# Kernel tuning notes

Measured on AMD Instinct MI355X. Metric: run time of the kernel, lower is better.

## Reference

```python
import jax, jax.numpy as jnp
import numpy as np

# MACE/molgym-style SimpleModel with max_ell=1, hidden_irreps = 64x0e + 64x1o,
# num_interactions=2, num_elements=10, num_bessel=8, polynomial cutoff p=5, r_max=5.0.
N, E, C, NE, NB, H = 20000, 320000, 64, 10, 8, 64
R_MAX = 5.0
P_CUT = 5


def _mlp(x, W1, W2, W3):
    # radial MLP producing per-edge tensor-product weights (silu nonlinearity)
    h = jax.nn.silu(x @ W1)
    h = jax.nn.silu(h @ W2)
    return h @ W3


def setup_inputs() -> dict:
    key = jax.random.key(0)
    ks = jax.random.split(key, 24)
    positions = jax.random.normal(ks[0], (N, 3), jnp.float32)
    edge_index = jax.random.randint(ks[1], (2, E), 0, N)
    shifts = jnp.zeros((E, 3), jnp.float32)
    species = jax.random.randint(ks[2], (N,), 0, NE)
    node_attrs = jax.nn.one_hot(species, NE, dtype=jnp.float32)

    def w(k, shape, fan_in):
        return jax.random.normal(k, shape, jnp.float32) / np.sqrt(fan_in)

    params = dict(
        W_embed=w(ks[3], (NE, C), NE),
        R1_W1=w(ks[4], (NB, H), NB), R1_W2=w(ks[5], (H, H), H), R1_W3=w(ks[6], (H, 2 * C), H),
        U1_s=w(ks[7], (C, C), C),
        L1_s=w(ks[8], (C, C), C), L1_v=w(ks[9], (C, C), C),
        K1_s=w(ks[10], (C, NE, C), C * NE),
        R2_W1=w(ks[11], (NB, H), NB), R2_W2=w(ks[12], (H, H), H), R2_W3=w(ks[13], (H, 4 * C), H),
        U2_s=w(ks[14], (C, C), C), U2_v=w(ks[15], (C, C), C),
        L2_s=w(ks[16], (2 * C, C), 2 * C), L2_v=w(ks[17], (2 * C, C), 2 * C),
        K2_s=w(ks[18], (C, NE, C), C * NE), K2_v=w(ks[19], (C, NE, C), C * NE),
    )
    return dict(positions=positions, node_attrs=node_attrs, edge_index=edge_index,
                shifts=shifts, **params)


def _forward(positions, node_attrs, shifts, W_embed,
             R1_W1, R1_W2, R1_W3, U1_s, L1_s, L1_v, K1_s,
             R2_W1, R2_W2, R2_W3, U2_s, U2_v, L2_s, L2_v, K2_s, K2_v,
             edge_index):
    snd, rcv = edge_index[0], edge_index[1]
    # edge vectors / lengths
    vec = positions[snd] - positions[rcv] + shifts            # [E,3]
    length = jnp.sqrt(jnp.sum(vec * vec, axis=1, keepdims=True) + 1e-12)  # [E,1]
    unit = vec / length
    # spherical harmonics (normalize=True, component normalization): Y0=1, Y1=sqrt(3)*r_hat
    Y1 = np.float32(np.sqrt(3.0)) * unit                      # [E,3]
    # Bessel radial basis * polynomial cutoff
    n = jnp.arange(1, NB + 1, dtype=jnp.float32)
    bessel = np.float32(np.sqrt(2.0 / R_MAX)) * jnp.sin(n * np.float32(np.pi) * length / R_MAX) / length
    u = length / R_MAX
    p = P_CUT
    poly = (1.0 - 0.5 * (p + 1) * (p + 2) * u ** p
            + p * (p + 2) * u ** (p + 1)
            - 0.5 * p * (p + 1) * u ** (p + 2))
    edge_feats = bessel * (poly * (u < 1.0))                  # [E,NB]
    # node embedding (linear on one-hot species)
    s0 = node_attrs @ W_embed                                 # [N,C]

    # ---- interaction block 1 (input feats: scalars only) ----
    s = s0 @ U1_s                                             # linear_up
    tpw = _mlp(edge_feats, R1_W1, R1_W2, R1_W3).reshape(E, 2, C)
    s_e = s[snd]                                              # gather sender feats
    m_s = tpw[:, 0] * s_e                                     # 0e x 0e -> 0e  [E,C]
    m_v = (tpw[:, 1] * s_e)[:, :, None] * Y1[:, None, :]      # 0e x 1o -> 1o  [E,C,3]
    agg_s = jax.ops.segment_sum(m_s, rcv, num_segments=N)
    agg_v = jax.ops.segment_sum(m_v, rcv, num_segments=N)
    skip_s = jnp.einsum('nu,nv,uvd->nd', s0, node_attrs, K1_s)  # skip tensor product
    s1 = agg_s @ L1_s + skip_s                                # [N,C]
    v1 = jnp.einsum('nci,cd->ndi', agg_v, L1_v)               # [N,C,3]

    # ---- interaction block 2 (input feats: 64x0e + 64x1o) ----
    s = s1 @ U2_s
    v = jnp.einsum('nci,cd->ndi', v1, U2_v)
    tpw = _mlp(edge_feats, R2_W1, R2_W2, R2_W3).reshape(E, 4, C)
    s_e, v_e = s[snd], v[snd]
    mA = tpw[:, 0] * s_e                                      # 0e x 0e -> 0e
    mB = (tpw[:, 1] * s_e)[:, :, None] * Y1[:, None, :]       # 0e x 1o -> 1o
    mC = tpw[:, 2][:, :, None] * v_e                          # 1o x 0e -> 1o
    mD = tpw[:, 3] * (jnp.einsum('eci,ei->ec', v_e, Y1) / np.float32(np.sqrt(3.0)))  # 1o x 1o -> 0e
    mid_s = jnp.concatenate([mA, mD], axis=1)                 # [E,2C]
    mid_v = jnp.concatenate([mB, mC], axis=1)                 # [E,2C,3]
    agg_s = jax.ops.segment_sum(mid_s, rcv, num_segments=N)
    agg_v = jax.ops.segment_sum(mid_v, rcv, num_segments=N)
    skip_s = jnp.einsum('nu,nv,uvd->nd', s1, node_attrs, K2_s)
    skip_v = jnp.einsum('nui,nv,uvd->ndi', v1, node_attrs, K2_v)
    s2 = agg_s @ L2_s + skip_s                                # [N,C]
    v2 = jnp.einsum('nci,cd->ndi', agg_v, L2_v) + skip_v      # [N,C,3]
    return jnp.concatenate([s2, v2.reshape(N, 3 * C)], axis=1)  # [N,4C]


def reference(positions, node_attrs, edge_index, shifts, W_embed,
              R1_W1, R1_W2, R1_W3, U1_s, L1_s, L1_v, K1_s,
              R2_W1, R2_W2, R2_W3, U2_s, U2_v, L2_s, L2_v, K2_s, K2_v):
    return _forward(positions, node_attrs, shifts, W_embed,
                    R1_W1, R1_W2, R1_W3, U1_s, L1_s, L1_v, K1_s,
                    R2_W1, R2_W2, R2_W3, U2_s, U2_v, L2_s, L2_v, K2_s, K2_v,
                    edge_index)
```

## Files before the change

### kernel.cpp

```cpp
#include <hip/hip_runtime.h>
#include <hip/hip_fp16.h>

#define NNODES 20000
#define NEDGES 320000
#define NELEM  10
#define NC     (NNODES * 64)

#define OFF_SUP1 ((size_t)0)
#define OFF_AGS1 ((size_t)1 * NC)
#define OFF_AGV1 ((size_t)2 * NC)
#define OFF_AGS2 ((size_t)0)
#define OFF_AGV2 ((size_t)2 * NC)
#define OFF_SUP2 ((size_t)8 * NC)
#define OFF_VUP2 ((size_t)9 * NC)
#define OFF_SKS2 ((size_t)12 * NC)
#define OFF_SKV2 ((size_t)13 * NC)
#define OFF_INT  ((size_t)16 * NC)

#define SMEM_BYTES 38656

typedef __attribute__((ext_vector_type(8))) short bf16x8;
typedef __attribute__((ext_vector_type(4))) float f32x4;

__device__ __forceinline__ float silu(float x) { return x / (1.0f + __expf(-x)); }
__device__ __forceinline__ int rfl(int v) { return __builtin_amdgcn_readfirstlane(v); }
__device__ __forceinline__ int rl_i(int v, int l) { return __builtin_amdgcn_readlane(v, l); }
__device__ __forceinline__ float rl_f(float v, int l) {
    return __int_as_float(__builtin_amdgcn_readlane(__float_as_int(v), l));
}
__device__ __forceinline__ uint2 split2(float x0, float x1) {
    unsigned int b0 = __float_as_uint(x0), b1 = __float_as_uint(x1);
    unsigned int h0 = (b0 + 0x7FFF + ((b0 >> 16) & 1)) & 0xFFFF0000u;
    unsigned int h1 = (b1 + 0x7FFF + ((b1 >> 16) & 1)) & 0xFFFF0000u;
    unsigned int l0 = __float_as_uint(x0 - __uint_as_float(h0));
    unsigned int l1 = __float_as_uint(x1 - __uint_as_float(h1));
    unsigned int hi = (h0 >> 16) | (h1 & 0xFFFF0000u);
    unsigned int lo = ((l0 + 0x7FFF + ((l0 >> 16) & 1)) >> 16)
                    | ((l1 + 0x7FFF + ((l1 >> 16) & 1)) & 0xFFFF0000u);
    return make_uint2(hi, lo);
}

__global__ __launch_bounds__(256) void k_wsplit(
    const float* __restrict__ W3a, const float* __restrict__ W3b,
    unsigned short* __restrict__ out)
{
    int t = blockIdx.x * 256 + threadIdx.x;
    float x; unsigned short *ph, *pl; int idx;
    if (t < 8192) {
        int n = t >> 6, k = t & 63;
        x = W3a[k * 128 + n]; ph = out; pl = out + 8192; idx = n * 64 + k;
    } else {
        int u = t - 8192; int n = u >> 6, k = u & 63;
        x = W3b[k * 256 + n]; ph = out + 16384; pl = out + 32768; idx = n * 64 + k;
    }
    unsigned int b = __float_as_uint(x);
    unsigned int h = (b + 0x7FFF + ((b >> 16) & 1)) & 0xFFFF0000u;
    unsigned int r = __float_as_uint(x - __uint_as_float(h));
    ph[idx] = (unsigned short)(h >> 16);
    pl[idx] = (unsigned short)((r + 0x7FFF + ((r >> 16) & 1)) >> 16);
}

__global__ __launch_bounds__(256) void k_hist(const int* __restrict__ eidx,
                                              int* __restrict__ hist)
{
    int e = blockIdx.x * 256 + threadIdx.x;
    atomicAdd(&hist[eidx[NEDGES + e]], 1);
}

__global__ __launch_bounds__(1024) void k_scan(const int* __restrict__ hist,
                                               int* __restrict__ cursor)
{
    __shared__ int wsum[16];
    __shared__ int gbase;
    int tid = threadIdx.x;
    int lane = tid & 63, wvid = tid >> 6;
    if (tid == 0) gbase = 0;
    __syncthreads();
    for (int seg = 0; seg < 20; ++seg) {
        int i = seg * 1024 + tid;
        int v = (i < NNODES) ? hist[i] : 0;
        int s = v;
        #pragma unroll
        for (int d = 1; d < 64; d <<= 1) {
            int t = __shfl_up(s, d, 64);
            if (lane >= d) s += t;
        }
        if (lane == 63) wsum[wvid] = s;
        __syncthreads();
        if (wvid == 0) {
            int w = (lane < 16) ? wsum[lane] : 0;
            #pragma unroll
            for (int d = 1; d < 16; d <<= 1) {
                int t = __shfl_up(w, d, 64);
                if (lane >= d) w += t;
            }
            if (lane < 16) wsum[lane] = w;
        }
        __syncthreads();
        int wbase = (wvid == 0) ? 0 : wsum[wvid - 1];
        if (i < NNODES) cursor[i] = gbase + wbase + s - v;
        int segtot = wsum[15];
        __syncthreads();
        if (tid == 0) gbase += segtot;
    }
}

__global__ __launch_bounds__(256) void k_scatter(const int* __restrict__ eidx,
                                                 int* __restrict__ cursor,
                                                 int* __restrict__ sorted)
{
    int e = blockIdx.x * 256 + threadIdx.x;
    int pos = atomicAdd(&cursor[eidx[NEDGES + e]], 1);
    sorted[pos] = e;
}

__global__ __launch_bounds__(256) void k_node_pre(
    const float* __restrict__ attrs, const float* __restrict__ Wemb,
    const float* __restrict__ U1s, __half* __restrict__ sUp1)
{
    int lane = threadIdx.x & 63, wv = threadIdx.x >> 6;
    int n = blockIdx.x * 4 + wv;
    __shared__ __align__(16) float s0sh[4][64];
    float s0 = 0.f;
    #pragma unroll
    for (int v = 0; v < NELEM; ++v) s0 += attrs[n * NELEM + v] * Wemb[v * 64 + lane];
    s0sh[wv][lane] = s0;
    __syncthreads();
    float a = 0.f;
    #pragma unroll 8
    for (int k = 0; k < 64; ++k) a += s0sh[wv][k] * U1s[k * 64 + lane];
    sUp1[n * 64 + lane] = __float2half_rn(a);
}

__global__ __launch_bounds__(256, 4) void k_edge1(
    const float* __restrict__ pos, const int* __restrict__ eidx,
    const float* __restrict__ shf, const int* __restrict__ sorted,
    const float* __restrict__ W1, const float* __restrict__ W2,
    const unsigned short* __restrict__ w3h, const unsigned short* __restrict__ w3l,
    const __half* __restrict__ sUp1,
    float* __restrict__ agS1, float* __restrict__ agV1)
{
    __shared__ __align__(16) char smem[SMEM_BYTES];
    float (*ysh)[3]   = (float (*)[3])(smem);
    int*  ssh         = (int*)(smem + 768);
    int*  rsh         = (int*)(smem + 1024);
    float (*h1sh)[65] = (float (*)[65])(smem + 1280);
    unsigned short (*h2buf)[64][72] = (unsigned short (*)[64][72])(smem + 17920);
    float (*fsh)[9]   = (float (*)[9])(smem + 36352);

    const int tid = threadIdx.x;
    const int lane = tid & 63;
    const int w = rfl(tid >> 6);
    const int e0 = blockIdx.x * 64;

    {
        int e = tid >> 2, sub = tid & 3;
        int sid = sorted[e0 + e];
        int snd = eidx[sid], rcv = eidx[NEDGES + sid];
        float dx = pos[snd * 3 + 0] - pos[rcv * 3 + 0] + shf[(size_t)sid * 3 + 0];
        float dy = pos[snd * 3 + 1] - pos[rcv * 3 + 1] + shf[(size_t)sid * 3 + 1];
        float dz = pos[snd * 3 + 2] - pos[rcv * 3 + 2] + shf[(size_t)sid * 3 + 2];
        float len = sqrtf(dx * dx + dy * dy + dz * dz + 1e-12f);
        float inv = 1.0f / len;
        float u = len * 0.2f;
        float u2 = u * u, u4 = u2 * u2, u5 = u4 * u, u6 = u5 * u, u7 = u6 * u;
        float cut = (u < 1.0f) ? (1.0f - 21.0f * u5 + 35.0f * u6 - 15.0f * u7) : 0.0f;
        float s = 0.632455532033676f * inv * cut;
        #pragma unroll
        for (int kk = 0; kk < 2; ++kk) {
            int k = sub * 2 + kk;
            fsh[e][k] = s * sinf((float)(k + 1) * 0.628318530717959f * len);
        }
        if (sub == 0) {
            ssh[e] = snd; rsh[e] = rcv;
            ysh[e][0] = 1.73205080756888f * dx * inv;
            ysh[e][1] = 1.73205080756888f * dy * inv;
            ysh[e][2] = 1.73205080756888f * dz * inv;
        }
    }
    __syncthreads();

    const int rAll = rsh[lane];
    const int sAll = ssh[lane];
    const float y0A = ysh[lane][0], y1A = ysh[lane][1], y2A = ysh[lane][2];

    {
        float f[8];
        #pragma unroll
        for (int k = 0; k < 8; ++k) f[k] = fsh[lane][k];
        const float* __restrict__ w1b = W1 + w * 16;
        #pragma unroll
        for (int j = 0; j < 16; ++j) {
            float a = 0.f;
            #pragma unroll
            for (int k = 0; k < 8; ++k) a = fmaf(f[k], w1b[k * 64 + j], a);
            h1sh[lane][w * 16 + j] = silu(a);
        }
    }
    __syncthreads();

    {
        const float2* __restrict__ w2b = (const float2*)W2 + w * 8;
        float2 acc[8];
        #pragma unroll
        for (int j = 0; j < 8; ++j) acc[j] = make_float2(0.f, 0.f);
        for (int k = 0; k < 64; ++k) {
            float h = h1sh[lane][k];
            const float2* __restrict__ wk = w2b + k * 32;
            #pragma unroll
            for (int j = 0; j < 8; ++j) {
                float2 wv = wk[j];
                acc[j].x = fmaf(h, wv.x, acc[j].x);
                acc[j].y = fmaf(h, wv.y, acc[j].y);
            }
        }
        #pragma unroll
        for (int j = 0; j < 8; ++j) {
            uint2 p = split2(silu(acc[j].x), silu(acc[j].y));
            *(unsigned int*)&h2buf[0][lane][w * 16 + 2 * j] = p.x;
            *(unsigned int*)&h2buf[1][lane][w * 16 + 2 * j] = p.y;
        }
    }
    __syncthreads();

    const int q = lane >> 4, nl = lane & 15;
    float* trw = (float*)(smem + 1280) + w * 1024;

    const unsigned short* ar = &h2buf[0][w * 16 + nl][0];
    const unsigned short* al = &h2buf[1][w * 16 + nl][0];
    bf16x8 ah0 = *(const bf16x8*)(ar + q * 8);
    bf16x8 ah1 = *(const bf16x8*)(ar + 32 + q * 8);
    bf16x8 al0 = *(const bf16x8*)(al + q * 8);
    bf16x8 al1 = *(const bf16x8*)(al + 32 + q * 8);

    float sreg[16];
    #pragma unroll
    for (int i = 0; i < 16; ++i)
        sreg[i] = __half2float(sUp1[rl_i(sAll, w * 16 + i) * 64 + lane]);

    #pragma unroll
    for (int nt = 0; nt < 4; ++nt) {
        int c = nt * 16 + nl;
        const unsigned short* wh = w3h + c * 64 + q * 8;
        const unsigned short* wl = w3l + c * 64 + q * 8;
        bf16x8 bh0 = *(const bf16x8*)wh;
        bf16x8 bh1 = *(const bf16x8*)(wh + 32);
        bf16x8 bl0 = *(const bf16x8*)wl;
        bf16x8 bl1 = *(const bf16x8*)(wl + 32);
        f32x4 a = {0.f, 0.f, 0.f, 0.f};
        a = __builtin_amdgcn_mfma_f32_16x16x32_bf16(ah0, bh0, a, 0, 0, 0);
        a = __builtin_amdgcn_mfma_f32_16x16x32_bf16(ah1, bh1, a, 0, 0, 0);
        a = __builtin_amdgcn_mfma_f32_16x16x32_bf16(ah0, bl0, a, 0, 0, 0);
        a = __builtin_amdgcn_mfma_f32_16x16x32_bf16(ah1, bl1, a, 0, 0, 0);
        a = __builtin_amdgcn_mfma_f32_16x16x32_bf16(al0, bh0, a, 0, 0, 0);
        a = __builtin_amdgcn_mfma_f32_16x16x32_bf16(al1, bh1, a, 0, 0, 0);
        #pragma unroll
        for (int r = 0; r < 4; ++r) {
            int li = q * 4 + r;
            trw[li * 64 + ((c + 4 * li) & 63)] = a[r];
        }
    }
    {
        float accS = 0.f;
        int cur = rl_i(rAll, w * 16);
        #pragma unroll
        for (int i = 0; i < 16; ++i) {
            int e = w * 16 + i;
            int rcv = rl_i(rAll, e);
            if (rcv != cur) {
                unsafeAtomicAdd(&agS1[cur * 64 + lane], accS);
                accS = 0.f; cur = rcv;
            }
            accS += trw[i * 64 + ((lane + 4 * i) & 63)] * sreg[i];
        }
        unsafeAtomicAdd(&agS1[cur * 64 + lane], accS);
    }

    #pragma unroll
    for (int nt = 0; nt < 4; ++nt) {
        int c = nt * 16 + nl;
        int ng = 64 + c;
        const unsigned short* wh = w3h + ng * 64 + q * 8;
        const unsigned short* wl = w3l + ng * 64 + q * 8;
        bf16x8 bh0 = *(const bf16x8*)wh;
        bf16x8 bh1 = *(const bf16x8*)(wh + 32);
        bf16x8 bl0 = *(const bf16x8*)wl;
        bf16x8 bl1 = *(const bf16x8*)(wl + 32);
        f32x4 a = {0.f, 0.f, 0.f, 0.f};
        a = __builtin_amdgcn_mfma_f32_16x16x32_bf16(ah0, bh0, a, 0, 0, 0);
        a = __builtin_amdgcn_mfma_f32_16x16x32_bf16(ah1, bh1, a, 0, 0, 0);
        a = __builtin_amdgcn_mfma_f32_16x16x32_bf16(ah0, bl0, a, 0, 0, 0);
        a = __builtin_amdgcn_mfma_f32_16x16x32_bf16(ah1, bl1, a, 0, 0, 0);
        a = __builtin_amdgcn_mfma_f32_16x16x32_bf16(al0, bh0, a, 0, 0, 0);
        a = __builtin_amdgcn_mfma_f32_16x16x32_bf16(al1, bh1, a, 0, 0, 0);
        #pragma unroll
        for (int r = 0; r < 4; ++r) {
            int li = q * 4 + r;
            trw[li * 64 + ((c + 4 * li) & 63)] = a[r];
        }
    }
    {
        float b0 = 0.f, b1 = 0.f, b2 = 0.f;
        int cur = rl_i(rAll, w * 16);
        #pragma unroll
        for (int i = 0; i < 16; ++i) {
            int e = w * 16 + i;
            int rcv = rl_i(rAll, e);
            if (rcv != cur) {
                unsafeAtomicAdd(&agV1[cur * 192 +       lane], b0);
                unsafeAtomicAdd(&agV1[cur * 192 +  64 + lane], b1);
                unsafeAtomicAdd(&agV1[cur * 192 + 128 + lane], b2);
                b0 = b1 = b2 = 0.f; cur = rcv;
            }
            float msg = trw[i * 64 + ((lane + 4 * i) & 63)] * sreg[i];
            b0 += msg * rl_f(y0A, e);
            b1 += msg * rl_f(y1A, e);
            b2 += msg * rl_f(y2A, e);
        }
        unsafeAtomicAdd(&agV1[cur * 192 +       lane], b0);
        unsafeAtomicAdd(&agV1[cur * 192 +  64 + lane], b1);
        unsafeAtomicAdd(&agV1[cur * 192 + 128 + lane], b2);
    }
}

__global__ __launch_bounds__(256) void k_node_mid(
    const float* __restrict__ attrs, const float* __restrict__ Wemb,
    const float* __restrict__ K1s, const float* __restrict__ L1s,
    const float* __restrict__ L1v,
    const float* __restrict__ U2s, const float* __restrict__ U2v,
    const float* __restrict__ K2s, const float* __restrict__ K2v,
    const float* __restrict__ agS1, const float* __restrict__ agV1,
    __half* __restrict__ sUp2, __half* __restrict__ vUp2,
    float* __restrict__ skS2, float* __restrict__ skV2)
{
    int lane = threadIdx.x & 63, wv = threadIdx.x >> 6;
    int n = blockIdx.x * 4 + wv;
    __shared__ float aSsh[4][64];
    __shared__ float aVsh[4][3][64];
    __shared__ float s0sh[4][64];
    __shared__ float s1sh[4][64];
    __shared__ float v1sh[4][3][64];

    int sp = 0;
    #pragma unroll
    for (int v = 0; v < NELEM; ++v) if (attrs[n * NELEM + v] > 0.5f) sp = v;
    aSsh[wv][lane] = agS1[n * 64 + lane];
    #pragma unroll
    for (int i = 0; i < 3; ++i) aVsh[wv][i][lane] = agV1[n * 192 + i * 64 + lane];
    s0sh[wv][lane] = Wemb[sp * 64 + lane];
    __syncthreads();

    float s1 = 0.f;
    #pragma unroll 8
    for (int k = 0; k < 64; ++k) s1 += aSsh[wv][k] * L1s[k * 64 + lane];
    #pragma unroll 8
    for (int k = 0; k < 64; ++k) s1 += s0sh[wv][k] * K1s[(k * NELEM + sp) * 64 + lane];
    float v1[3] = {0.f, 0.f, 0.f};
    #pragma unroll 8
    for (int k = 0; k < 64; ++k) {
        float w = L1v[k * 64 + lane];
        v1[0] += aVsh[wv][0][k] * w;
        v1[1] += aVsh[wv][1][k] * w;
        v1[2] += aVsh[wv][2][k] * w;
    }
    s1sh[wv][lane] = s1;
    #pragma unroll
    for (int i = 0; i < 3; ++i) v1sh[wv][i][lane] = v1[i];
    __syncthreads();

    float su = 0.f, ks = 0.f;
    float vu[3] = {0.f, 0.f, 0.f}, kv[3] = {0.f, 0.f, 0.f};
    #pragma unroll 8
    for (int k = 0; k < 64; ++k) su += s1sh[wv][k] * U2s[k * 64 + lane];
    #pragma unroll 8
    for (int k = 0; k < 64; ++k) ks += s1sh[wv][k] * K2s[(k * NELEM + sp) * 64 + lane];
    #pragma unroll 8
    for (int k = 0; k < 64; ++k) {
        float w = U2v[k * 64 + lane];
        vu[0] += v1sh[wv][0][k] * w;
        vu[1] += v1sh[wv][1][k] * w;
        vu[2] += v1sh[wv][2][k] * w;
    }
    #pragma unroll 8
    for (int k = 0; k < 64; ++k) {
        float w = K2v[(k * NELEM + sp) * 64 + lane];
        kv[0] += v1sh[wv][0][k] * w;
        kv[1] += v1sh[wv][1][k] * w;
        kv[2] += v1sh[wv][2][k] * w;
    }
    sUp2[n * 64 + lane] = __float2half_rn(su);
    skS2[n * 64 + lane] = ks;
    #pragma unroll
    for (int i = 0; i < 3; ++i) {
        vUp2[n * 192 + i * 64 + lane] = __float2half_rn(vu[i]);
        skV2[n * 192 + i * 64 + lane] = kv[i];
    }
}

__global__ __launch_bounds__(256, 4) void k_edge2(
    const float* __restrict__ pos, const int* __restrict__ eidx,
    const float* __restrict__ shf, const int* __restrict__ sorted,
    const float* __restrict__ W1, const float* __restrict__ W2,
    const unsigned short* __restrict__ w3h, const unsigned short* __restrict__ w3l,
    const __half* __restrict__ sUp2, const __half* __restrict__ vUp2,
    float* __restrict__ agS2, float* __restrict__ agV2)
{
    __shared__ __align__(16) char smem[SMEM_BYTES];
    float (*ysh)[3]   = (float (*)[3])(smem);
    int*  ssh         = (int*)(smem + 768);
    int*  rsh         = (int*)(smem + 1024);
    float (*h1sh)[65] = (float (*)[65])(smem + 1280);
    unsigned short (*h2buf)[64][72] = (unsigned short (*)[64][72])(smem + 17920);
    float (*fsh)[9]   = (float (*)[9])(smem + 36352);

    const int tid = threadIdx.x;
    const int lane = tid & 63;
    const int w = rfl(tid >> 6);
    const int e0 = blockIdx.x * 64;

    {
        int e = tid >> 2, sub = tid & 3;
        int sid = sorted[e0 + e];
        int snd = eidx[sid], rcv = eidx[NEDGES + sid];
        float dx = pos[snd * 3 + 0] - pos[rcv * 3 + 0] + shf[(size_t)sid * 3 + 0];
        float dy = pos[snd * 3 + 1] - pos[rcv * 3 + 1] + shf[(size_t)sid * 3 + 1];
        float dz = pos[snd * 3 + 2] - pos[rcv * 3 + 2] + shf[(size_t)sid * 3 + 2];
        float len = sqrtf(dx * dx + dy * dy + dz * dz + 1e-12f);
        float inv = 1.0f / len;
        float u = len * 0.2f;
        float u2 = u * u, u4 = u2 * u2, u5 = u4 * u, u6 = u5 * u, u7 = u6 * u;
        float cut = (u < 1.0f) ? (1.0f - 21.0f * u5 + 35.0f * u6 - 15.0f * u7) : 0.0f;
        float s = 0.632455532033676f * inv * cut;
        #pragma unroll
        for (int kk = 0; kk < 2; ++kk) {
            int k = sub * 2 + kk;
            fsh[e][k] = s * sinf((float)(k + 1) * 0.628318530717959f * len);
        }
        if (sub == 0) {
            ssh[e] = snd; rsh[e] = rcv;
            ysh[e][0] = 1.73205080756888f * dx * inv;
            ysh[e][1] = 1.73205080756888f * dy * inv;
            ysh[e][2] = 1.73205080756888f * dz * inv;
        }
    }
    __syncthreads();

    const int rAll = rsh[lane];
    const int sAll = ssh[lane];
    const float y0A = ysh[lane][0], y1A = ysh[lane][1], y2A = ysh[lane][2];

    {
        float f[8];
        #pragma unroll
        for (int k = 0; k < 8; ++k) f[k] = fsh[lane][k];
        const float* __restrict__ w1b = W1 + w * 16;
        #pragma unroll
        for (int j = 0; j < 16; ++j) {
            float a = 0.f;
            #pragma unroll
            for (int k = 0; k < 8; ++k) a = fmaf(f[k], w1b[k * 64 + j], a);
            h1sh[lane][w * 16 + j] = silu(a);
        }
    }
    __syncthreads();

    {
        const float2* __restrict__ w2b = (const float2*)W2 + w * 8;
        float2 acc[8];
        #pragma unroll
        for (int j = 0; j < 8; ++j) acc[j] = make_float2(0.f, 0.f);
        for (int k = 0; k < 64; ++k) {
            float h = h1sh[lane][k];
            const float2* __restrict__ wk = w2b + k * 32;
            #pragma unroll
            for (int j = 0; j < 8; ++j) {
                float2 wv = wk[j];
                acc[j].x = fmaf(h, wv.x, acc[j].x);
                acc[j].y = fmaf(h, wv.y, acc[j].y);
            }
        }
        #pragma unroll
        for (int j = 0; j < 8; ++j) {
            uint2 p = split2(silu(acc[j].x), silu(acc[j].y));
            *(unsigned int*)&h2buf[0][lane][w * 16 + 2 * j] = p.x;
            *(unsigned int*)&h2buf[1][lane][w * 16 + 2 * j] = p.y;
        }
    }
    __syncthreads();

    const int q = lane >> 4, nl = lane & 15;
    float* trw = (float*)(smem + 1280) + w * 1024;

    const unsigned short* ar = &h2buf[0][w * 16 + nl][0];
    const unsigned short* al = &h2buf[1][w * 16 + nl][0];
    bf16x8 ah0 = *(const bf16x8*)(ar + q * 8);
    bf16x8 ah1 = *(const bf16x8*)(ar + 32 + q * 8);
    bf16x8 al0 = *(const bf16x8*)(al + q * 8);
    bf16x8 al1 = *(const bf16x8*)(al + 32 + q * 8);

    float sreg[16];
    #pragma unroll
    for (int i = 0; i < 16; ++i)
        sreg[i] = __half2float(sUp2[rl_i(sAll, w * 16 + i) * 64 + lane]);

    #pragma unroll
    for (int nt = 0; nt < 4; ++nt) {
        int c = nt * 16 + nl;
        const unsigned short* wh = w3h + c * 64 + q * 8;
        const unsigned short* wl = w3l + c * 64 + q * 8;
        bf16x8 bh0 = *(const bf16x8*)wh;
        bf16x8 bh1 = *(const bf16x8*)(wh + 32);
        bf16x8 bl0 = *(const bf16x8*)wl;
        bf16x8 bl1 = *(const bf16x8*)(wl + 32);
        f32x4 a = {0.f, 0.f, 0.f, 0.f};
        a = __builtin_amdgcn_mfma_f32_16x16x32_bf16(ah0, bh0, a, 0, 0, 0);
        a = __builtin_amdgcn_mfma_f32_16x16x32_bf16(ah1, bh1, a, 0, 0, 0);
        a = __builtin_amdgcn_mfma_f32_16x16x32_bf16(ah0, bl0, a, 0, 0, 0);
        a = __builtin_amdgcn_mfma_f32_16x16x32_bf16(ah1, bl1, a, 0, 0, 0);
        a = __builtin_amdgcn_mfma_f32_16x16x32_bf16(al0, bh0, a, 0, 0, 0);
        a = __builtin_amdgcn_mfma_f32_16x16x32_bf16(al1, bh1, a, 0, 0, 0);
        #pragma unroll
        for (int r = 0; r < 4; ++r) {
            int li = q * 4 + r;
            trw[li * 64 + ((c + 4 * li) & 63)] = a[r];
        }
    }
    {
        float accS = 0.f;
        int cur = rl_i(rAll, w * 16);
        #pragma unroll
        for (int i = 0; i < 16; ++i) {
            int e = w * 16 + i;
            int rcv = rl_i(rAll, e);
            if (rcv != cur) {
                unsafeAtomicAdd(&agS2[cur * 128 + lane], accS);
                accS = 0.f; cur = rcv;
            }
            accS += trw[i * 64 + ((lane + 4 * i) & 63)] * sreg[i];
        }
        unsafeAtomicAdd(&agS2[cur * 128 + lane], accS);
    }

    #pragma unroll
    for (int nt = 0; nt < 4; ++nt) {
        int c = nt * 16 + nl;
        int ng = 64 + c;
        const unsigned short* wh = w3h + ng * 64 + q * 8;
        const unsigned short* wl = w3l + ng * 64 + q * 8;
        bf16x8 bh0 = *(const bf16x8*)wh;
        bf16x8 bh1 = *(const bf16x8*)(wh + 32);
        bf16x8 bl0 = *(const bf16x8*)wl;
        bf16x8 bl1 = *(const bf16x8*)(wl + 32);
        f32x4 a = {0.f, 0.f, 0.f, 0.f};
        a = __builtin_amdgcn_mfma_f32_16x16x32_bf16(ah0, bh0, a, 0, 0, 0);
        a = __builtin_amdgcn_mfma_f32_16x16x32_bf16(ah1, bh1, a, 0, 0, 0);
        a = __builtin_amdgcn_mfma_f32_16x16x32_bf16(ah0, bl0, a, 0, 0, 0);
        a = __builtin_amdgcn_mfma_f32_16x16x32_bf16(ah1, bl1, a, 0, 0, 0);
        a = __builtin_amdgcn_mfma_f32_16x16x32_bf16(al0, bh0, a, 0, 0, 0);
        a = __builtin_amdgcn_mfma_f32_16x16x32_bf16(al1, bh1, a, 0, 0, 0);
        #pragma unroll
        for (int r = 0; r < 4; ++r) {
            int li = q * 4 + r;
            trw[li * 64 + ((c + 4 * li) & 63)] = a[r];
        }
    }
    {
        float b0 = 0.f, b1 = 0.f, b2 = 0.f;
        int cur = rl_i(rAll, w * 16);
        #pragma unroll
        for (int i = 0; i < 16; ++i) {
            int e = w * 16 + i;
            int rcv = rl_i(rAll, e);
            if (rcv != cur) {
                unsafeAtomicAdd(&agV2[cur * 384 + 0 * 128 + lane], b0);
                unsafeAtomicAdd(&agV2[cur * 384 + 1 * 128 + lane], b1);
                unsafeAtomicAdd(&agV2[cur * 384 + 2 * 128 + lane], b2);
                b0 = b1 = b2 = 0.f; cur = rcv;
            }
            float msg = trw[i * 64 + ((lane + 4 * i) & 63)] * sreg[i];
            b0 += msg * rl_f(y0A, e);
            b1 += msg * rl_f(y1A, e);
            b2 += msg * rl_f(y2A, e);
        }
        unsafeAtomicAdd(&agV2[cur * 384 + 0 * 128 + lane], b0);
        unsafeAtomicAdd(&agV2[cur * 384 + 1 * 128 + lane], b1);
        unsafeAtomicAdd(&agV2[cur * 384 + 2 * 128 + lane], b2);
    }

    float vr0[16], vr1[16], vr2[16];
    #pragma unroll
    for (int i = 0; i < 16; ++i) {
        int snd = rl_i(sAll, w * 16 + i);
        vr0[i] = __half2float(vUp2[snd * 192 +       lane]);
        vr1[i] = __half2float(vUp2[snd * 192 +  64 + lane]);
        vr2[i] = __half2float(vUp2[snd * 192 + 128 + lane]);
    }

    #pragma unroll
    for (int nt = 0; nt < 4; ++nt) {
        int c = nt * 16 + nl;
        int ng = 128 + c;
        const unsigned short* wh = w3h + ng * 64 + q * 8;
        const unsigned short* wl = w3l + ng * 64 + q * 8;
        bf16x8 bh0 = *(const bf16x8*)wh;
        bf16x8 bh1 = *(const bf16x8*)(wh + 32);
        bf16x8 bl0 = *(const bf16x8*)wl;
        bf16x8 bl1 = *(const bf16x8*)(wl + 32);
        f32x4 a = {0.f, 0.f, 0.f, 0.f};
        a = __builtin_amdgcn_mfma_f32_16x16x32_bf16(ah0, bh0, a, 0, 0, 0);
        a = __builtin_amdgcn_mfma_f32_16x16x32_bf16(ah1, bh1, a, 0, 0, 0);
        a = __builtin_amdgcn_mfma_f32_16x16x32_bf16(ah0, bl0, a, 0, 0, 0);
        a = __builtin_amdgcn_mfma_f32_16x16x32_bf16(ah1, bl1, a, 0, 0, 0);
        a = __builtin_amdgcn_mfma_f32_16x16x32_bf16(al0, bh0, a, 0, 0, 0);
        a = __builtin_amdgcn_mfma_f32_16x16x32_bf16(al1, bh1, a, 0, 0, 0);
        #pragma unroll
        for (int r = 0; r < 4; ++r) {
            int li = q * 4 + r;
            trw[li * 64 + ((c + 4 * li) & 63)] = a[r];
        }
    }
    {
        float c0 = 0.f, c1 = 0.f, c2 = 0.f;
        int cur = rl_i(rAll, w * 16);
        #pragma unroll
        for (int i = 0; i < 16; ++i) {
            int e = w * 16 + i;
            int rcv = rl_i(rAll, e);
            if (rcv != cur) {
                unsafeAtomicAdd(&agV2[cur * 384 + 0 * 128 + 64 + lane], c0);
                unsafeAtomicAdd(&agV2[cur * 384 + 1 * 128 + 64 + lane], c1);
                unsafeAtomicAdd(&agV2[cur * 384 + 2 * 128 + 64 + lane], c2);
                c0 = c1 = c2 = 0.f; cur = rcv;
            }
            float tvC = trw[i * 64 + ((lane + 4 * i) & 63)];
            c0 += tvC * vr0[i];
            c1 += tvC * vr1[i];
            c2 += tvC * vr2[i];
        }
        unsafeAtomicAdd(&agV2[cur * 384 + 0 * 128 + 64 + lane], c0);
        unsafeAtomicAdd(&agV2[cur * 384 + 1 * 128 + 64 + lane], c1);
        unsafeAtomicAdd(&agV2[cur * 384 + 2 * 128 + 64 + lane], c2);
    }

    #pragma unroll
    for (int nt = 0; nt < 4; ++nt) {
        int c = nt * 16 + nl;
        int ng = 192 + c;
        const unsigned short* wh = w3h + ng * 64 + q * 8;
        const unsigned short* wl = w3l + ng * 64 + q * 8;
        bf16x8 bh0 = *(const bf16x8*)wh;
        bf16x8 bh1 = *(const bf16x8*)(wh + 32);
        bf16x8 bl0 = *(const bf16x8*)wl;
        bf16x8 bl1 = *(const bf16x8*)(wl + 32);
        f32x4 a = {0.f, 0.f, 0.f, 0.f};
        a = __builtin_amdgcn_mfma_f32_16x16x32_bf16(ah0, bh0, a, 0, 0, 0);
        a = __builtin_amdgcn_mfma_f32_16x16x32_bf16(ah1, bh1, a, 0, 0, 0);
        a = __builtin_amdgcn_mfma_f32_16x16x32_bf16(ah0, bl0, a, 0, 0, 0);
        a = __builtin_amdgcn_mfma_f32_16x16x32_bf16(ah1, bl1, a, 0, 0, 0);
        a = __builtin_amdgcn_mfma_f32_16x16x32_bf16(al0, bh0, a, 0, 0, 0);
        a = __builtin_amdgcn_mfma_f32_16x16x32_bf16(al1, bh1, a, 0, 0, 0);
        #pragma unroll
        for (int r = 0; r < 4; ++r) {
            int li = q * 4 + r;
            trw[li * 64 + ((c + 4 * li) & 63)] = a[r];
        }
    }
    {
        float accD = 0.f;
        int cur = rl_i(rAll, w * 16);
        #pragma unroll
        for (int i = 0; i < 16; ++i) {
            int e = w * 16 + i;
            int rcv = rl_i(rAll, e);
            if (rcv != cur) {
                unsafeAtomicAdd(&agS2[cur * 128 + 64 + lane], accD);
                accD = 0.f; cur = rcv;
            }
            float tvD = trw[i * 64 + ((lane + 4 * i) & 63)];
            float dotvy = vr0[i] * rl_f(y0A, e) + vr1[i] * rl_f(y1A, e)
                        + vr2[i] * rl_f(y2A, e);
            accD += tvD * dotvy * 0.577350269189626f;
        }
        unsafeAtomicAdd(&agS2[cur * 128 + 64 + lane], accD);
    }
}

__global__ __launch_bounds__(256) void k_node_out(
    const float* __restrict__ L2s, const float* __restrict__ L2v,
    const float* __restrict__ agS2, const float* __restrict__ agV2,
    const float* __restrict__ skS2, const float* __restrict__ skV2,
    float* __restrict__ out)
{
    int lane = threadIdx.x & 63, wv = threadIdx.x >> 6;
    int n = blockIdx.x * 4 + wv;
    __shared__ __align__(16) float aS[4][128];
    __shared__ __align__(16) float aV[4][3][128];

    aS[wv][lane]      = agS2[n * 128 + lane];
    aS[wv][64 + lane] = agS2[n * 128 + 64 + lane];
    #pragma unroll
    for (int i = 0; i < 3; ++i) {
        aV[wv][i][lane]      = agV2[n * 384 + i * 128 + lane];
        aV[wv][i][64 + lane] = agV2[n * 384 + i * 128 + 64 + lane];
    }
    __syncthreads();

    float s2 = skS2[n * 64 + lane];
    #pragma unroll 8
    for (int u = 0; u < 128; ++u) s2 += aS[wv][u] * L2s[u * 64 + lane];
    float v2[3];
    #pragma unroll
    for (int i = 0; i < 3; ++i) v2[i] = skV2[n * 192 + i * 64 + lane];
    #pragma unroll 8
    for (int u = 0; u < 128; ++u) {
        float w = L2v[u * 64 + lane];
        v2[0] += aV[wv][0][u] * w;
        v2[1] += aV[wv][1][u] * w;
        v2[2] += aV[wv][2][u] * w;
    }
    out[(size_t)n * 256 + lane] = s2;
    #pragma unroll
    for (int i = 0; i < 3; ++i)
        out[(size_t)n * 256 + 64 + lane * 3 + i] = v2[i];
}

extern "C" void kernel_launch(void* const* d_in, const int* in_sizes, int n_in,
                              void* d_out, int out_size, void* d_ws, size_t ws_size,
                              hipStream_t stream)
{
    (void)in_sizes; (void)n_in; (void)out_size; (void)ws_size;
    const float* positions  = (const float*)d_in[0];
    const float* node_attrs = (const float*)d_in[1];
    const int*   edge_index = (const int*)d_in[2];
    const float* shifts     = (const float*)d_in[3];
    const float* W_embed    = (const float*)d_in[4];
    const float* R1W1 = (const float*)d_in[5];
    const float* R1W2 = (const float*)d_in[6];
    const float* R1W3 = (const float*)d_in[7];
    const float* U1s  = (const float*)d_in[8];
    const float* L1s  = (const float*)d_in[9];
    const float* L1v  = (const float*)d_in[10];
    const float* K1s  = (const float*)d_in[11];
    const float* R2W1 = (const float*)d_in[12];
    const float* R2W2 = (const float*)d_in[13];
    const float* R2W3 = (const float*)d_in[14];
    const float* U2s  = (const float*)d_in[15];
    const float* U2v  = (const float*)d_in[16];
    const float* L2s  = (const float*)d_in[17];
    const float* L2v  = (const float*)d_in[18];
    const float* K2s  = (const float*)d_in[19];
    const float* K2v  = (const float*)d_in[20];

    float* wsf = (float*)d_ws;
    int*   wsi = (int*)(wsf + OFF_INT);
    int* hist   = wsi;
    int* cursor = wsi + 20000;
    int* sorted = wsi + 40000;
    unsigned short* wsh = (unsigned short*)(wsi + 360000);
    const unsigned short* w3a_hi = wsh;
    const unsigned short* w3a_lo = wsh + 8192;
    const unsigned short* w3b_hi = wsh + 16384;
    const unsigned short* w3b_lo = wsh + 32768;

    __half* sUp1h = (__half*)(wsf + OFF_SUP1);
    __half* sUp2h = (__half*)(wsf + OFF_SUP2);
    __half* vUp2h = (__half*)(wsf + OFF_VUP2);

    hipMemsetAsync(wsf + OFF_AGS1, 0, (size_t)4 * NC * sizeof(float), stream);
    hipMemsetAsync(hist, 0, 20000 * sizeof(int), stream);

    k_wsplit<<<96, 256, 0, stream>>>(R1W3, R2W3, wsh);
    k_hist<<<NEDGES / 256, 256, 0, stream>>>(edge_index, hist);
    k_scan<<<1, 1024, 0, stream>>>(hist, cursor);
    k_scatter<<<NEDGES / 256, 256, 0, stream>>>(edge_index, cursor, sorted);

    k_node_pre<<<NNODES / 4, 256, 0, stream>>>(node_attrs, W_embed, U1s, sUp1h);
    k_edge1<<<NEDGES / 64, 256, 0, stream>>>(positions, edge_index, shifts, sorted,
                                             R1W1, R1W2, w3a_hi, w3a_lo,
                                             sUp1h, wsf + OFF_AGS1, wsf + OFF_AGV1);
    k_node_mid<<<NNODES / 4, 256, 0, stream>>>(node_attrs, W_embed, K1s, L1s, L1v,
                                               U2s, U2v, K2s, K2v,
                                               wsf + OFF_AGS1, wsf + OFF_AGV1,
                                               sUp2h, vUp2h,
                                               wsf + OFF_SKS2, wsf + OFF_SKV2);
    hipMemsetAsync(wsf + OFF_AGS2, 0, (size_t)8 * NC * sizeof(float), stream);
    k_edge2<<<NEDGES / 64, 256, 0, stream>>>(positions, edge_index, shifts, sorted,
                                             R2W1, R2W2, w3b_hi, w3b_lo,
                                             sUp2h, vUp2h,
                                             wsf + OFF_AGS2, wsf + OFF_AGV2);
    k_node_out<<<NNODES / 4, 256, 0, stream>>>(L2s, L2v, wsf + OFF_AGS2, wsf + OFF_AGV2,
                                               wsf + OFF_SKS2, wsf + OFF_SKV2,
                                               (float*)d_out);
}
```

Before: 620.2 us.

## Accumulate edge aggregations in packed fp16 atomics and swizzle edge blocks across XCDs

Result: no change. 624.9 us (+0.8%).

```diff
diff --git a/kernel.cpp b/kernel.cpp
--- a/kernel.cpp
+++ b/kernel.cpp
@@ -19,6 +19,10 @@
 
 #define SMEM_BYTES 38656
 
+__device__ __forceinline__ int xcd_swz(int bid) {
+    return (bid & 7) * 625 + (bid >> 3);
+}
+
 typedef __attribute__((ext_vector_type(8))) short bf16x8;
 typedef __attribute__((ext_vector_type(4))) float f32x4;
 
@@ -40,6 +44,14 @@
     return make_uint2(hi, lo);
 }
 
+__device__ __forceinline__ void flush2(__half* base, int lane, float v) {
+    float p = __shfl_xor(v, 1);
+    if (!(lane & 1)) {
+        __half2 h2 = __halves2half2(__float2half_rn(v), __float2half_rn(p));
+        unsafeAtomicAdd((__half2*)(base + lane), h2);
+    }
+}
+
 __global__ __launch_bounds__(256) void k_wsplit(
     const float* __restrict__ W3a, const float* __restrict__ W3b,
     unsigned short* __restrict__ out)
@@ -138,7 +150,7 @@
     const float* __restrict__ W1, const float* __restrict__ W2,
     const unsigned short* __restrict__ w3h, const unsigned short* __restrict__ w3l,
     const __half* __restrict__ sUp1,
-    float* __restrict__ agS1, float* __restrict__ agV1)
+    __half* __restrict__ agS1, __half* __restrict__ agV1)
 {
     __shared__ __align__(16) char smem[SMEM_BYTES];
     float (*ysh)[3]   = (float (*)[3])(smem);
@@ -151,7 +163,7 @@
     const int tid = threadIdx.x;
     const int lane = tid & 63;
     const int w = rfl(tid >> 6);
-    const int e0 = blockIdx.x * 64;
+    const int e0 = xcd_swz(blockIdx.x) * 64;
 
     {
         int e = tid >> 2, sub = tid & 3;
@@ -268,12 +280,12 @@
             int e = w * 16 + i;
             int rcv = rl_i(rAll, e);
             if (rcv != cur) {
-                unsafeAtomicAdd(&agS1[cur * 64 + lane], accS);
+                flush2(agS1 + cur * 64, lane, accS);
                 accS = 0.f; cur = rcv;
             }
             accS += trw[i * 64 + ((lane + 4 * i) & 63)] * sreg[i];
         }
-        unsafeAtomicAdd(&agS1[cur * 64 + lane], accS);
+        flush2(agS1 + cur * 64, lane, accS);
     }
 
     #pragma unroll
@@ -307,9 +319,9 @@
             int e = w * 16 + i;
             int rcv = rl_i(rAll, e);
             if (rcv != cur) {
-                unsafeAtomicAdd(&agV1[cur * 192 +       lane], b0);
-                unsafeAtomicAdd(&agV1[cur * 192 +  64 + lane], b1);
-                unsafeAtomicAdd(&agV1[cur * 192 + 128 + lane], b2);
+                flush2(agV1 + cur * 192,       lane, b0);
+                flush2(agV1 + cur * 192 +  64, lane, b1);
+                flush2(agV1 + cur * 192 + 128, lane, b2);
                 b0 = b1 = b2 = 0.f; cur = rcv;
             }
             float msg = trw[i * 64 + ((lane + 4 * i) & 63)] * sreg[i];
@@ -317,9 +329,9 @@
             b1 += msg * rl_f(y1A, e);
             b2 += msg * rl_f(y2A, e);
         }
-        unsafeAtomicAdd(&agV1[cur * 192 +       lane], b0);
-        unsafeAtomicAdd(&agV1[cur * 192 +  64 + lane], b1);
-        unsafeAtomicAdd(&agV1[cur * 192 + 128 + lane], b2);
+        flush2(agV1 + cur * 192,       lane, b0);
+        flush2(agV1 + cur * 192 +  64, lane, b1);
+        flush2(agV1 + cur * 192 + 128, lane, b2);
     }
 }
 
@@ -329,7 +341,7 @@
     const float* __restrict__ L1v,
     const float* __restrict__ U2s, const float* __restrict__ U2v,
     const float* __restrict__ K2s, const float* __restrict__ K2v,
-    const float* __restrict__ agS1, const float* __restrict__ agV1,
+    const __half* __restrict__ agS1, const __half* __restrict__ agV1,
     __half* __restrict__ sUp2, __half* __restrict__ vUp2,
     float* __restrict__ skS2, float* __restrict__ skV2)
 {
@@ -344,9 +356,10 @@
     int sp = 0;
     #pragma unroll
     for (int v = 0; v < NELEM; ++v) if (attrs[n * NELEM + v] > 0.5f) sp = v;
-    aSsh[wv][lane] = agS1[n * 64 + lane];
-    #pragma unroll
-    for (int i = 0; i < 3; ++i) aVsh[wv][i][lane] = agV1[n * 192 + i * 64 + lane];
+    aSsh[wv][lane] = __half2float(agS1[n * 64 + lane]);
+    #pragma unroll
+    for (int i = 0; i < 3; ++i)
+        aVsh[wv][i][lane] = __half2float(agV1[n * 192 + i * 64 + lane]);
     s0sh[wv][lane] = Wemb[sp * 64 + lane];
     __syncthreads();
 
@@ -403,7 +416,7 @@
     const float* __restrict__ W1, const float* __restrict__ W2,
     const unsigned short* __restrict__ w3h, const unsigned short* __restrict__ w3l,
     const __half* __restrict__ sUp2, const __half* __restrict__ vUp2,
-    float* __restrict__ agS2, float* __restrict__ agV2)
+    __half* __restrict__ agS2, __half* __restrict__ agV2)
 {
     __shared__ __align__(16) char smem[SMEM_BYTES];
     float (*ysh)[3]   = (float (*)[3])(smem);
@@ -416,7 +429,7 @@
     const int tid = threadIdx.x;
     const int lane = tid & 63;
     const int w = rfl(tid >> 6);
-    const int e0 = blockIdx.x * 64;
+    const int e0 = xcd_swz(blockIdx.x) * 64;
 
     {
         int e = tid >> 2, sub = tid & 3;
@@ -533,12 +546,12 @@
             int e = w * 16 + i;
             int rcv = rl_i(rAll, e);
             if (rcv != cur) {
-                unsafeAtomicAdd(&agS2[cur * 128 + lane], accS);
+                flush2(agS2 + cur * 128, lane, accS);
                 accS = 0.f; cur = rcv;
             }
             accS += trw[i * 64 + ((lane + 4 * i) & 63)] * sreg[i];
         }
-        unsafeAtomicAdd(&agS2[cur * 128 + lane], accS);
+        flush2(agS2 + cur * 128, lane, accS);
     }
 
     #pragma unroll
@@ -572,9 +585,9 @@
             int e = w * 16 + i;
             int rcv = rl_i(rAll, e);
             if (rcv != cur) {
-                unsafeAtomicAdd(&agV2[cur * 384 + 0 * 128 + lane], b0);
-                unsafeAtomicAdd(&agV2[cur * 384 + 1 * 128 + lane], b1);
-                unsafeAtomicAdd(&agV2[cur * 384 + 2 * 128 + lane], b2);
+                flush2(agV2 + cur * 384,       lane, b0);
+                flush2(agV2 + cur * 384 + 128, lane, b1);
+                flush2(agV2 + cur * 384 + 256, lane, b2);
                 b0 = b1 = b2 = 0.f; cur = rcv;
             }
             float msg = trw[i * 64 + ((lane + 4 * i) & 63)] * sreg[i];
@@ -582,9 +595,9 @@
             b1 += msg * rl_f(y1A, e);
             b2 += msg * rl_f(y2A, e);
         }
-        unsafeAtomicAdd(&agV2[cur * 384 + 0 * 128 + lane], b0);
-        unsafeAtomicAdd(&agV2[cur * 384 + 1 * 128 + lane], b1);
-        unsafeAtomicAdd(&agV2[cur * 384 + 2 * 128 + lane], b2);
+        flush2(agV2 + cur * 384,       lane, b0);
+        flush2(agV2 + cur * 384 + 128, lane, b1);
+        flush2(agV2 + cur * 384 + 256, lane, b2);
     }
 
     float vr0[16], vr1[16], vr2[16];
@@ -627,9 +640,9 @@
             int e = w * 16 + i;
             int rcv = rl_i(rAll, e);
             if (rcv != cur) {
-                unsafeAtomicAdd(&agV2[cur * 384 + 0 * 128 + 64 + lane], c0);
-                unsafeAtomicAdd(&agV2[cur * 384 + 1 * 128 + 64 + lane], c1);
-                unsafeAtomicAdd(&agV2[cur * 384 + 2 * 128 + 64 + lane], c2);
+                flush2(agV2 + cur * 384 +  64, lane, c0);
+                flush2(agV2 + cur * 384 + 192, lane, c1);
+                flush2(agV2 + cur * 384 + 320, lane, c2);
                 c0 = c1 = c2 = 0.f; cur = rcv;
             }
             float tvC = trw[i * 64 + ((lane + 4 * i) & 63)];
@@ -637,9 +650,9 @@
             c1 += tvC * vr1[i];
             c2 += tvC * vr2[i];
         }
-        unsafeAtomicAdd(&agV2[cur * 384 + 0 * 128 + 64 + lane], c0);
-        unsafeAtomicAdd(&agV2[cur * 384 + 1 * 128 + 64 + lane], c1);
-        unsafeAtomicAdd(&agV2[cur * 384 + 2 * 128 + 64 + lane], c2);
+        flush2(agV2 + cur * 384 +  64, lane, c0);
+        flush2(agV2 + cur * 384 + 192, lane, c1);
+        flush2(agV2 + cur * 384 + 320, lane, c2);
     }
 
     #pragma unroll
@@ -673,7 +686,7 @@
             int e = w * 16 + i;
             int rcv = rl_i(rAll, e);
             if (rcv != cur) {
-                unsafeAtomicAdd(&agS2[cur * 128 + 64 + lane], accD);
+                flush2(agS2 + cur * 128 + 64, lane, accD);
                 accD = 0.f; cur = rcv;
             }
             float tvD = trw[i * 64 + ((lane + 4 * i) & 63)];
@@ -681,13 +694,13 @@
                         + vr2[i] * rl_f(y2A, e);
             accD += tvD * dotvy * 0.577350269189626f;
         }
-        unsafeAtomicAdd(&agS2[cur * 128 + 64 + lane], accD);
+        flush2(agS2 + cur * 128 + 64, lane, accD);
     }
 }
 
 __global__ __launch_bounds__(256) void k_node_out(
     const float* __restrict__ L2s, const float* __restrict__ L2v,
-    const float* __restrict__ agS2, const float* __restrict__ agV2,
+    const __half* __restrict__ agS2, const __half* __restrict__ agV2,
     const float* __restrict__ skS2, const float* __restrict__ skV2,
     float* __restrict__ out)
 {
@@ -696,12 +709,12 @@
     __shared__ __align__(16) float aS[4][128];
     __shared__ __align__(16) float aV[4][3][128];
 
-    aS[wv][lane]      = agS2[n * 128 + lane];
-    aS[wv][64 + lane] = agS2[n * 128 + 64 + lane];
+    aS[wv][lane]      = __half2float(agS2[n * 128 + lane]);
+    aS[wv][64 + lane] = __half2float(agS2[n * 128 + 64 + lane]);
     #pragma unroll
     for (int i = 0; i < 3; ++i) {
-        aV[wv][i][lane]      = agV2[n * 384 + i * 128 + lane];
-        aV[wv][i][64 + lane] = agV2[n * 384 + i * 128 + 64 + lane];
+        aV[wv][i][lane]      = __half2float(agV2[n * 384 + i * 128 + lane]);
+        aV[wv][i][64 + lane] = __half2float(agV2[n * 384 + i * 128 + 64 + lane]);
     }
     __syncthreads();
 
@@ -765,8 +778,14 @@
     __half* sUp1h = (__half*)(wsf + OFF_SUP1);
     __half* sUp2h = (__half*)(wsf + OFF_SUP2);
     __half* vUp2h = (__half*)(wsf + OFF_VUP2);
-
-    hipMemsetAsync(wsf + OFF_AGS1, 0, (size_t)4 * NC * sizeof(float), stream);
+    __half* agS1h = (__half*)(wsf + OFF_AGS1);
+    __half* agV1h = (__half*)(wsf + OFF_AGV1);
+    __half* agS2h = (__half*)(wsf + OFF_AGS2);
+    __half* agV2h = (__half*)(wsf + OFF_AGV2);
+
+    hipMemsetAsync(wsf + OFF_AGS1, 0,
+                   (size_t)NC * sizeof(float) + (size_t)20000 * 192 * sizeof(__half),
+                   stream);
     hipMemsetAsync(hist, 0, 20000 * sizeof(int), stream);
 
     k_wsplit<<<96, 256, 0, stream>>>(R1W3, R2W3, wsh);
@@ -777,18 +796,20 @@
     k_node_pre<<<NNODES / 4, 256, 0, stream>>>(node_attrs, W_embed, U1s, sUp1h);
     k_edge1<<<NEDGES / 64, 256, 0, stream>>>(positions, edge_index, shifts, sorted,
                                              R1W1, R1W2, w3a_hi, w3a_lo,
-                                             sUp1h, wsf + OFF_AGS1, wsf + OFF_AGV1);
+                                             sUp1h, agS1h, agV1h);
     k_node_mid<<<NNODES / 4, 256, 0, stream>>>(node_attrs, W_embed, K1s, L1s, L1v,
                                                U2s, U2v, K2s, K2v,
-                                               wsf + OFF_AGS1, wsf + OFF_AGV1,
+                                               agS1h, agV1h,
                                                sUp2h, vUp2h,
                                                wsf + OFF_SKS2, wsf + OFF_SKV2);
-    hipMemsetAsync(wsf + OFF_AGS2, 0, (size_t)8 * NC * sizeof(float), stream);
+    hipMemsetAsync(wsf + OFF_AGS2, 0,
+                   (size_t)2 * NC * sizeof(float) + (size_t)20000 * 384 * sizeof(__half),
+                   stream);
     k_edge2<<<NEDGES / 64, 256, 0, stream>>>(positions, edge_index, shifts, sorted,
                                              R2W1, R2W2, w3b_hi, w3b_lo,
                                              sUp2h, vUp2h,
-                                             wsf + OFF_AGS2, wsf + OFF_AGV2);
-    k_node_out<<<NNODES / 4, 256, 0, stream>>>(L2s, L2v, wsf + OFF_AGS2, wsf + OFF_AGV2,
+                                             agS2h, agV2h);
+    k_node_out<<<NNODES / 4, 256, 0, stream>>>(L2s, L2v, agS2h, agV2h,
                                                wsf + OFF_SKS2, wsf + OFF_SKV2,
                                                (float*)d_out);
 }
```
